# Performance work log

Hardware: AMD Instinct MI355X
Metric: run time of the kernel (lower is better)

The kernel has to match this reference:

```python
import jax, jax.numpy as jnp
import numpy as np

N_NODES = 50000
N_EDGES = 640000
N_GRAPHS = 64
D_IN = 3
D_H = 128
N_CLASSES = 10
EPS = 1e-5


def setup_inputs() -> dict:
    key = jax.random.key(0)
    ks = jax.random.split(key, 32)
    inp = {
        "x": jax.random.normal(ks[0], (N_NODES, D_IN), dtype=jnp.float32),
        "src": jax.random.randint(ks[1], (N_EDGES,), 0, N_NODES, dtype=jnp.int32),
        "dst": jax.random.randint(ks[2], (N_EDGES,), 0, N_NODES, dtype=jnp.int32),
        "batch": jnp.sort(jax.random.randint(ks[3], (N_NODES,), 0, N_GRAPHS, dtype=jnp.int32)),
        "enc_w": jax.random.normal(ks[4], (D_IN, D_H), dtype=jnp.float32) * 0.1,
        "enc_b": jnp.zeros((D_H,), jnp.float32),
        "fc_w": jax.random.normal(ks[5], (D_H, D_H), dtype=jnp.float32) * 0.05,
        "fc_b": jnp.zeros((D_H,), jnp.float32),
        "pred_w": jax.random.normal(ks[6], (D_H, N_CLASSES), dtype=jnp.float32) * 0.05,
        "pred_b": jnp.zeros((N_CLASSES,), jnp.float32),
    }
    for i in range(4):
        inp[f"w{i}"] = jax.random.normal(ks[8 + i], (D_H, D_H), dtype=jnp.float32) * 0.05
        inp[f"b{i}"] = jnp.zeros((D_H,), jnp.float32)
        inp[f"ln_w{i}"] = jnp.ones((D_H,), jnp.float32)
        inp[f"ln_b{i}"] = jnp.zeros((D_H,), jnp.float32)
    return inp


def _gcn_norm(src, dst, n):
    # add self-loops, symmetric deg^{-1/2} normalization (GCNConv default)
    loop = jnp.arange(n, dtype=src.dtype)
    src_f = jnp.concatenate([src, loop])
    dst_f = jnp.concatenate([dst, loop])
    deg = jax.ops.segment_sum(jnp.ones_like(dst_f, jnp.float32), dst_f, num_segments=n)
    dinv = jnp.where(deg > 0, 1.0 / jnp.sqrt(deg), 0.0)
    norm = dinv[src_f] * dinv[dst_f]
    return src_f, dst_f, norm


def _gcn(x, w, b, src_f, dst_f, norm, n):
    h = x @ w                           # [N, D]
    m = h[src_f] * norm[:, None]        # gather + scale  [E+N, D]
    return jax.ops.segment_sum(m, dst_f, num_segments=n) + b


def _graph_ln(x, w, b):
    # PyG LayerNorm mode='graph', batch=None: normalize over ALL nodes+channels
    mu = x.mean()
    sd = jnp.sqrt(((x - mu) ** 2).mean())
    return (x - mu) / (sd + EPS) * w + b


def reference(x, src, dst, batch, enc_w, enc_b, fc_w, fc_b, pred_w, pred_b,
              w0, b0, ln_w0, ln_b0, w1, b1, ln_w1, ln_b1,
              w2, b2, ln_w2, ln_b2, w3, b3, ln_w3, ln_b3):
    n = x.shape[0]
    src_f, dst_f, norm = _gcn_norm(src, dst, n)
    h = jax.nn.elu(x @ enc_w + enc_b)   # input encoder (Linear + ELU)
    convs = [(w0, b0, ln_w0, ln_b0), (w1, b1, ln_w1, ln_b1),
             (w2, b2, ln_w2, ln_b2), (w3, b3, ln_w3, ln_b3)]
    for w, b, lw, lb in convs:
        h = _gcn(h, w, b, src_f, dst_f, norm, n)
        h = jax.nn.relu(h)
        h = _graph_ln(h, lw, lb)
    g = jax.ops.segment_max(h, batch, num_segments=N_GRAPHS)  # global_max_pool
    g = jnp.tanh(g @ fc_w + fc_b)
    return g @ pred_w + pred_b
```

## Files before the change

### kernel.cpp

```cpp
#include <hip/hip_runtime.h>
#include <cfloat>
#include <cmath>

#define D 128
#define D4 32
#define LB 64

typedef __attribute__((ext_vector_type(8))) short short8;
typedef __attribute__((ext_vector_type(4))) float f32x4;

__device__ __forceinline__ float4 f4fma(float s, float4 a, float4 acc) {
    acc.x = fmaf(s, a.x, acc.x);
    acc.y = fmaf(s, a.y, acc.y);
    acc.z = fmaf(s, a.z, acc.z);
    acc.w = fmaf(s, a.w, acc.w);
    return acc;
}

__device__ __forceinline__ unsigned short f2bf(float x) {
    unsigned int b = __float_as_uint(x);
    unsigned int r = (b + 0x7FFFu + ((b >> 16) & 1u)) >> 16;
    return (unsigned short)r;
}

__device__ __forceinline__ unsigned int pack2bf(float a, float b) {
    return (unsigned int)f2bf(a) | ((unsigned int)f2bf(b) << 16);
}

__device__ __forceinline__ float bf2f(unsigned short u) {
    return __uint_as_float(((unsigned int)u) << 16);
}

__device__ __forceinline__ void accum8(float* a, float nrm, uint4 t) {
    a[0] = fmaf(nrm, bf2f((unsigned short)(t.x & 0xFFFFu)), a[0]);
    a[1] = fmaf(nrm, bf2f((unsigned short)(t.x >> 16)), a[1]);
    a[2] = fmaf(nrm, bf2f((unsigned short)(t.y & 0xFFFFu)), a[2]);
    a[3] = fmaf(nrm, bf2f((unsigned short)(t.y >> 16)), a[3]);
    a[4] = fmaf(nrm, bf2f((unsigned short)(t.z & 0xFFFFu)), a[4]);
    a[5] = fmaf(nrm, bf2f((unsigned short)(t.z >> 16)), a[5]);
    a[6] = fmaf(nrm, bf2f((unsigned short)(t.w & 0xFFFFu)), a[6]);
    a[7] = fmaf(nrm, bf2f((unsigned short)(t.w >> 16)), a[7]);
}

__global__ void k_count(const int* __restrict__ dst, int* __restrict__ cnt, int E) {
    int i = blockIdx.x * blockDim.x + threadIdx.x;
    if (i < E) atomicAdd(&cnt[dst[i]], 1);
}

__global__ void k_scan1(const int* __restrict__ cnt, int* __restrict__ bsum, int N) {
    __shared__ int red[256];
    int i = blockIdx.x * 256 + threadIdx.x;
    red[threadIdx.x] = (i < N) ? cnt[i] : 0;
    __syncthreads();
    for (int off = 128; off; off >>= 1) {
        if (threadIdx.x < off) red[threadIdx.x] += red[threadIdx.x + off];
        __syncthreads();
    }
    if (threadIdx.x == 0) bsum[blockIdx.x] = red[0];
}

__global__ void k_scan2(int* __restrict__ bsum, int NB, int* __restrict__ rowptrN) {
    __shared__ int s[256];
    int t = threadIdx.x;
    int v = (t < NB) ? bsum[t] : 0;
    s[t] = v;
    __syncthreads();
    for (int off = 1; off < 256; off <<= 1) {
        int u = (t >= off) ? s[t - off] : 0;
        __syncthreads();
        s[t] += u;
        __syncthreads();
    }
    if (t < NB) bsum[t] = (t == 0) ? 0 : s[t - 1];
    if (t == 255) *rowptrN = s[255];
}

__global__ void k_scan3(const int* __restrict__ cnt, const int* __restrict__ bsum,
                        int* __restrict__ rowptr, int* __restrict__ cur,
                        float* __restrict__ dinv, int N) {
    __shared__ int s[256];
    int i = blockIdx.x * 256 + threadIdx.x;
    int v = (i < N) ? cnt[i] : 0;
    s[threadIdx.x] = v;
    __syncthreads();
    for (int off = 1; off < 256; off <<= 1) {
        int u = (threadIdx.x >= off) ? s[threadIdx.x - off] : 0;
        __syncthreads();
        s[threadIdx.x] += u;
        __syncthreads();
    }
    if (i < N) {
        int excl = ((threadIdx.x == 0) ? 0 : s[threadIdx.x - 1]) + bsum[blockIdx.x];
        rowptr[i] = excl;
        cur[i] = excl;
        dinv[i] = 1.0f / sqrtf((float)v + 1.0f);
    }
}

__global__ void k_fill(const int* __restrict__ src, const int* __restrict__ dst,
                       const float* __restrict__ dinv, int* __restrict__ cur,
                       int2* __restrict__ edata, int E) {
    int e = blockIdx.x * blockDim.x + threadIdx.x;
    if (e >= E) return;
    int s = src[e], d = dst[e];
    int p = atomicAdd(&cur[d], 1);
    edata[p] = make_int2(s, __float_as_int(dinv[s] * dinv[d]));
}

__global__ void k_enc(const float* __restrict__ x, const float* __restrict__ w,
                      const float* __restrict__ b, unsigned short* __restrict__ h, int N) {
    int idx = blockIdx.x * blockDim.x + threadIdx.x;
    if (idx >= N * D4) return;
    int n = idx >> 5, c4 = idx & 31;
    const float4* w4 = (const float4*)w;
    float4 b4 = ((const float4*)b)[c4];
    float x0 = x[n * 3 + 0], x1 = x[n * 3 + 1], x2 = x[n * 3 + 2];
    float4 v = b4;
    v = f4fma(x0, w4[0 * D4 + c4], v);
    v = f4fma(x1, w4[1 * D4 + c4], v);
    v = f4fma(x2, w4[2 * D4 + c4], v);
    v.x = v.x > 0.f ? v.x : expm1f(v.x);
    v.y = v.y > 0.f ? v.y : expm1f(v.y);
    v.z = v.z > 0.f ? v.z : expm1f(v.z);
    v.w = v.w > 0.f ? v.w : expm1f(v.w);
    ushort4 o;
    o.x = f2bf(v.x); o.y = f2bf(v.y); o.z = f2bf(v.z); o.w = f2bf(v.w);
    ((ushort4*)h)[idx] = o;
}

__global__ void k_prep(const float* __restrict__ w, const float* __restrict__ lw,
                       const float* __restrict__ lb, const double* __restrict__ sums,
                       unsigned short* __restrict__ wt, float* __restrict__ konst, int N) {
    __shared__ float sc[D], of[D];
    float mu = 0.f, inv = 1.f;
    if (lw) {
        double M = (double)N * D;
        double m = sums[0] / M;
        double var = sums[1] / M - m * m;
        float sd = sqrtf(var > 0.0 ? (float)var : 0.f);
        inv = 1.f / (sd + 1e-5f);
        mu = (float)m;
    }
    for (int i = threadIdx.x; i < D; i += blockDim.x) {
        float l = lw ? lw[i] : 1.f;
        float s = inv * l;
        sc[i] = s;
        of[i] = (lw ? lb[i] : 0.f) - mu * s;
    }
    __syncthreads();
    if (blockIdx.x < 8) {
        int nl = threadIdx.x & 15;
        int ck = threadIdx.x >> 4;
        int n = blockIdx.x * 16 + nl;
        unsigned int p[4];
        #pragma unroll
        for (int q = 0; q < 4; ++q) {
            int k0 = ck * 8 + 2 * q;
            float v0 = sc[k0 + 0] * w[(k0 + 0) * D + n];
            float v1 = sc[k0 + 1] * w[(k0 + 1) * D + n];
            p[q] = pack2bf(v0, v1);
        }
        uint4 u = make_uint4(p[0], p[1], p[2], p[3]);
        ((uint4*)(wt + (size_t)n * D))[ck] = u;
    } else {
        for (int j = threadIdx.x; j < D; j += blockDim.x) {
            float acc = 0.f;
            for (int c = 0; c < D; ++c) acc = fmaf(of[c], w[c * D + j], acc);
            konst[j] = acc;
        }
    }
}

__launch_bounds__(256)
__global__ void k_layer(const unsigned short* __restrict__ Ain,
                        const unsigned short* __restrict__ wt,
                        const float* __restrict__ konst, const float* __restrict__ bias,
                        const int2* __restrict__ edata, const int* __restrict__ rowptr,
                        const float* __restrict__ dinv,
                        unsigned short* __restrict__ Aout,
                        double* __restrict__ sums, int N) {
    __shared__ uint4 a_lds4[1024];
    __shared__ float rs[LB];
    __shared__ float ss[4], sq[4];
    char* a_lds = (char*)a_lds4;
    int row0 = blockIdx.x * LB;

    int g = threadIdx.x >> 4;
    int lane = threadIdx.x & 15;
    const uint4* T16 = (const uint4*)Ain;
    for (int k = 0; k < 4; ++k) {
        int nl = g * 4 + k;
        int n = row0 + nl;
        if (n < N) {
            int e0 = rowptr[n], e1 = rowptr[n + 1];
            float acc[8];
            #pragma unroll
            for (int q = 0; q < 8; ++q) acc[q] = 0.f;
            float rsum = 0.f;
            int e = e0;
            for (; e + 8 <= e1; e += 8) {
                int2 ed[8]; uint4 tv[8];
                #pragma unroll
                for (int j = 0; j < 8; ++j) ed[j] = edata[e + j];
                #pragma unroll
                for (int j = 0; j < 8; ++j) tv[j] = T16[(size_t)ed[j].x * 16 + lane];
                #pragma unroll
                for (int j = 0; j < 8; ++j) {
                    float nm = __int_as_float(ed[j].y);
                    accum8(acc, nm, tv[j]);
                    rsum += nm;
                }
            }
            for (; e + 4 <= e1; e += 4) {
                int2 ed[4]; uint4 tv[4];
                #pragma unroll
                for (int j = 0; j < 4; ++j) ed[j] = edata[e + j];
                #pragma unroll
                for (int j = 0; j < 4; ++j) tv[j] = T16[(size_t)ed[j].x * 16 + lane];
                #pragma unroll
                for (int j = 0; j < 4; ++j) {
                    float nm = __int_as_float(ed[j].y);
                    accum8(acc, nm, tv[j]);
                    rsum += nm;
                }
            }
            for (; e < e1; ++e) {
                int2 d = edata[e];
                float nm = __int_as_float(d.y);
                accum8(acc, nm, T16[(size_t)d.x * 16 + lane]);
                rsum += nm;
            }
            float di = dinv[n];
            float sl = di * di;
            accum8(acc, sl, T16[(size_t)n * 16 + lane]);
            rsum += sl;
            int i = nl * 16 + lane;
            int byte = (i << 4) ^ ((nl & 7) << 4);
            *(uint4*)(a_lds + byte) = make_uint4(pack2bf(acc[0], acc[1]),
                                                 pack2bf(acc[2], acc[3]),
                                                 pack2bf(acc[4], acc[5]),
                                                 pack2bf(acc[6], acc[7]));
            if (lane == 0) rs[nl] = rsum;
        }
    }
    __syncthreads();

    int wv = threadIdx.x >> 6;
    int l64 = threadIdx.x & 63;
    int lrow = l64 & 15;
    int kg = l64 >> 4;

    f32x4 acc2[8];
    #pragma unroll
    for (int ct = 0; ct < 8; ++ct) acc2[ct] = (f32x4){0.f, 0.f, 0.f, 0.f};

    #pragma unroll
    for (int ks = 0; ks < 4; ++ks) {
        int ar = wv * 16 + lrow;
        int abyte = (ar * 256 + ks * 64 + kg * 16) ^ ((ar & 7) << 4);
        short8 a = *(short8*)(a_lds + abyte);
        #pragma unroll
        for (int ct = 0; ct < 8; ++ct) {
            int wr = ct * 16 + lrow;
            short8 b = *(const short8*)(wt + (size_t)wr * D + ks * 32 + kg * 8);
            acc2[ct] = __builtin_amdgcn_mfma_f32_16x16x32_bf16(a, b, acc2[ct], 0, 0, 0);
        }
    }

    float ls = 0.f, lq = 0.f;
    #pragma unroll
    for (int ct = 0; ct < 8; ++ct) {
        int col = ct * 16 + lrow;
        float kc = konst[col];
        float bb = bias[col];
        #pragma unroll
        for (int r = 0; r < 4; ++r) {
            int rtile = wv * 16 + kg * 4 + r;
            int row = row0 + rtile;
            if (row < N) {
                float v = acc2[ct][r] + rs[rtile] * kc + bb;
                v = fmaxf(v, 0.f);
                Aout[(size_t)row * D + col] = f2bf(v);
                ls += v;
                lq += v * v;
            }
        }
    }
    for (int off = 32; off; off >>= 1) {
        ls += __shfl_down(ls, off);
        lq += __shfl_down(lq, off);
    }
    if (l64 == 0) { ss[wv] = ls; sq[wv] = lq; }
    __syncthreads();
    if (threadIdx.x == 0) {
        float S = ss[0] + ss[1] + ss[2] + ss[3];
        float Q = sq[0] + sq[1] + sq[2] + sq[3];
        atomicAdd(&sums[0], (double)S);
        atomicAdd(&sums[1], (double)Q);
    }
}

__launch_bounds__(512)
__global__ void k_tail(const unsigned short* __restrict__ A, const int* __restrict__ batch,
                       const float* __restrict__ lw, const float* __restrict__ lb,
                       const double* __restrict__ sums,
                       const float* __restrict__ fc_w, const float* __restrict__ fc_b,
                       const float* __restrict__ pred_w, const float* __restrict__ pred_b,
                       float* __restrict__ out, int N) {
    int gi = blockIdx.x;
    int lo = 0, hi = N;
    while (lo < hi) { int mid = (lo + hi) >> 1; if (batch[mid] < gi) lo = mid + 1; else hi = mid; }
    int start = lo;
    hi = N;
    while (lo < hi) { int mid = (lo + hi) >> 1; if (batch[mid] < gi + 1) lo = mid + 1; else hi = mid; }
    int end = lo;

    int c = threadIdx.x & 127, sub = threadIdx.x >> 7;
    double M = (double)N * D;
    double m_ = sums[0] / M;
    double var = sums[1] / M - m_ * m_;
    float sd = sqrtf(var > 0.0 ? (float)var : 0.f);
    float inv = 1.f / (sd + 1e-5f);
    float s = inv * lw[c];
    float o = lb[c] - (float)m_ * s;

    float mx = -FLT_MAX;
    for (int node = start + sub; node < end; node += 4)
        mx = fmaxf(mx, fmaf(bf2f(A[(size_t)node * D + c]), s, o));

    __shared__ float red[4][128];
    __shared__ float gm[128], tr[128];
    red[sub][c] = mx;
    __syncthreads();
    if (sub == 0)
        gm[c] = fmaxf(fmaxf(red[0][c], red[1][c]), fmaxf(red[2][c], red[3][c]));
    __syncthreads();
    if (threadIdx.x < 128) {
        float acc = fc_b[c];
        for (int k = 0; k < D; ++k) acc = fmaf(gm[k], fc_w[k * D + c], acc);
        tr[c] = tanhf(acc);
    }
    __syncthreads();
    if (threadIdx.x < 10) {
        int j = threadIdx.x;
        float acc = pred_b[j];
        for (int k = 0; k < D; ++k) acc = fmaf(tr[k], pred_w[k * 10 + j], acc);
        out[gi * 10 + j] = acc;
    }
}

extern "C" void kernel_launch(void* const* d_in, const int* in_sizes, int n_in,
                              void* d_out, int out_size, void* d_ws, size_t ws_size,
                              hipStream_t stream) {
    const float* x      = (const float*)d_in[0];
    const int*   src    = (const int*)d_in[1];
    const int*   dst    = (const int*)d_in[2];
    const int*   batch  = (const int*)d_in[3];
    const float* enc_w  = (const float*)d_in[4];
    const float* enc_b  = (const float*)d_in[5];
    const float* fc_w   = (const float*)d_in[6];
    const float* fc_b   = (const float*)d_in[7];
    const float* pred_w = (const float*)d_in[8];
    const float* pred_b = (const float*)d_in[9];

    int N = in_sizes[0] / 3;
    int E = in_sizes[1];
    int G = out_size / 10;
    int NB = (N + 255) / 256;

    char* ws = (char*)d_ws;
    size_t off = 0;
    auto align512 = [](size_t v) { return (v + 511) / 512 * 512; };
    int*   cnt    = (int*)(ws + off);   off += align512((size_t)N * 4);
    double* sums  = (double*)(ws + off); off += 512;
    float* dinv   = (float*)(ws + off); off += align512((size_t)N * 4);
    int*   rowptr = (int*)(ws + off);   off += align512(((size_t)N + 1) * 4);
    int*   cur    = (int*)(ws + off);   off += align512((size_t)N * 4);
    int*   bsum   = (int*)(ws + off);   off += align512(1024);
    int2*  edata  = (int2*)(ws + off);  off += align512((size_t)E * 8);
    unsigned short* A0 = (unsigned short*)(ws + off); off += align512((size_t)N * D * 2);
    unsigned short* A1 = (unsigned short*)(ws + off); off += align512((size_t)N * D * 2);
    unsigned short* wt = (unsigned short*)(ws + off); off += align512((size_t)D * D * 2);
    float* konst  = (float*)(ws + off); off += align512((size_t)D * 4);

    hipMemsetAsync(cnt, 0, align512((size_t)N * 4) + 512, stream);
    k_count<<<(E + 255) / 256, 256, 0, stream>>>(dst, cnt, E);
    k_scan1<<<NB, 256, 0, stream>>>(cnt, bsum, N);
    k_scan2<<<1, 256, 0, stream>>>(bsum, NB, rowptr + N);
    k_scan3<<<NB, 256, 0, stream>>>(cnt, bsum, rowptr, cur, dinv, N);
    k_fill<<<(E + 255) / 256, 256, 0, stream>>>(src, dst, dinv, cur, edata, E);

    int tot4 = N * D4;
    k_enc<<<(tot4 + 255) / 256, 256, 0, stream>>>(x, enc_w, enc_b, A0, N);

    int NBL = (N + LB - 1) / LB;
    unsigned short* Ain = A0;
    unsigned short* Aout = A1;
    for (int L = 0; L < 4; ++L) {
        const float* w  = (const float*)d_in[10 + 4 * L];
        const float* b  = (const float*)d_in[11 + 4 * L];
        const float* lwp = L ? (const float*)d_in[12 + 4 * (L - 1)] : nullptr;
        const float* lbp = L ? (const float*)d_in[13 + 4 * (L - 1)] : nullptr;
        k_prep<<<9, 256, 0, stream>>>(w, lwp, lbp, &sums[2 * (L ? L - 1 : 0)], wt, konst, N);
        k_layer<<<NBL, 256, 0, stream>>>(Ain, wt, konst, b, edata, rowptr, dinv,
                                         Aout, &sums[2 * L], N);
        unsigned short* tmp = Ain; Ain = Aout; Aout = tmp;
    }

    const float* lw3 = (const float*)d_in[12 + 4 * 3];
    const float* lb3 = (const float*)d_in[13 + 4 * 3];
    k_tail<<<G, 512, 0, stream>>>(Ain, batch, lw3, lb3, &sums[6],
                                  fc_w, fc_b, pred_w, pred_b, (float*)d_out, N);
}
```

Before: 567.4 us.

## Halve layer block rows and merge three-pass scan into one kernel

The fused GCN layer kernel now handles 32 rows per block instead of 64. The four waves split the MFMA work as two row tiles by two 64-column halves, which doubles the block count and halves LDS use to raise occupancy and parallelism on the gather. The three scan kernels are replaced by one kernel in which each block recomputes its prefix by summing all earlier counts, removing two launches. The cost is redundant quadratic reads of the count array and more repeated weight loads per row.

```diff
diff --git a/kernel.cpp b/kernel.cpp
--- a/kernel.cpp
+++ b/kernel.cpp
@@ -4,7 +4,7 @@
 
 #define D 128
 #define D4 32
-#define LB 64
+#define LB 32
 
 typedef __attribute__((ext_vector_type(8))) short short8;
 typedef __attribute__((ext_vector_type(4))) float f32x4;
@@ -47,54 +47,39 @@
     if (i < E) atomicAdd(&cnt[dst[i]], 1);
 }
 
-__global__ void k_scan1(const int* __restrict__ cnt, int* __restrict__ bsum, int N) {
-    __shared__ int red[256];
-    int i = blockIdx.x * 256 + threadIdx.x;
-    red[threadIdx.x] = (i < N) ? cnt[i] : 0;
+__global__ void k_scanall(const int* __restrict__ cnt, int* __restrict__ rowptr,
+                          int* __restrict__ cur, float* __restrict__ dinv,
+                          int N, int NB) {
+    __shared__ int pre[256];
+    int b = blockIdx.x, t = threadIdx.x;
+    int limit = b * 256;
+    int s = 0;
+    for (int i = t; i < limit; i += 256) s += cnt[i];
+    pre[t] = s;
     __syncthreads();
     for (int off = 128; off; off >>= 1) {
-        if (threadIdx.x < off) red[threadIdx.x] += red[threadIdx.x + off];
+        if (t < off) pre[t] += pre[t + off];
         __syncthreads();
     }
-    if (threadIdx.x == 0) bsum[blockIdx.x] = red[0];
-}
-
-__global__ void k_scan2(int* __restrict__ bsum, int NB, int* __restrict__ rowptrN) {
-    __shared__ int s[256];
-    int t = threadIdx.x;
-    int v = (t < NB) ? bsum[t] : 0;
-    s[t] = v;
+    int base = pre[0];
+    __syncthreads();
+    int i = b * 256 + t;
+    int v = (i < N) ? cnt[i] : 0;
+    pre[t] = v;
     __syncthreads();
     for (int off = 1; off < 256; off <<= 1) {
-        int u = (t >= off) ? s[t - off] : 0;
+        int u = (t >= off) ? pre[t - off] : 0;
         __syncthreads();
-        s[t] += u;
+        pre[t] += u;
         __syncthreads();
     }
-    if (t < NB) bsum[t] = (t == 0) ? 0 : s[t - 1];
-    if (t == 255) *rowptrN = s[255];
-}
-
-__global__ void k_scan3(const int* __restrict__ cnt, const int* __restrict__ bsum,
-                        int* __restrict__ rowptr, int* __restrict__ cur,
-                        float* __restrict__ dinv, int N) {
-    __shared__ int s[256];
-    int i = blockIdx.x * 256 + threadIdx.x;
-    int v = (i < N) ? cnt[i] : 0;
-    s[threadIdx.x] = v;
-    __syncthreads();
-    for (int off = 1; off < 256; off <<= 1) {
-        int u = (threadIdx.x >= off) ? s[threadIdx.x - off] : 0;
-        __syncthreads();
-        s[threadIdx.x] += u;
-        __syncthreads();
-    }
     if (i < N) {
-        int excl = ((threadIdx.x == 0) ? 0 : s[threadIdx.x - 1]) + bsum[blockIdx.x];
+        int excl = base + ((t == 0) ? 0 : pre[t - 1]);
         rowptr[i] = excl;
         cur[i] = excl;
         dinv[i] = 1.0f / sqrtf((float)v + 1.0f);
     }
+    if (b == NB - 1 && t == 255) rowptr[N] = base + pre[255];
 }
 
 __global__ void k_fill(const int* __restrict__ src, const int* __restrict__ dst,
@@ -179,7 +164,7 @@
                         const float* __restrict__ dinv,
                         unsigned short* __restrict__ Aout,
                         double* __restrict__ sums, int N) {
-    __shared__ uint4 a_lds4[1024];
+    __shared__ uint4 a_lds4[512];
     __shared__ float rs[LB];
     __shared__ float ss[4], sq[4];
     char* a_lds = (char*)a_lds4;
@@ -188,8 +173,8 @@
     int g = threadIdx.x >> 4;
     int lane = threadIdx.x & 15;
     const uint4* T16 = (const uint4*)Ain;
-    for (int k = 0; k < 4; ++k) {
-        int nl = g * 4 + k;
+    for (int k = 0; k < 2; ++k) {
+        int nl = g * 2 + k;
         int n = row0 + nl;
         if (n < N) {
             int e0 = rowptr[n], e1 = rowptr[n + 1];
@@ -249,33 +234,35 @@
     int l64 = threadIdx.x & 63;
     int lrow = l64 & 15;
     int kg = l64 >> 4;
-
-    f32x4 acc2[8];
+    int rt = wv & 1;
+    int cb = wv >> 1;
+
+    f32x4 acc2[4];
     #pragma unroll
-    for (int ct = 0; ct < 8; ++ct) acc2[ct] = (f32x4){0.f, 0.f, 0.f, 0.f};
+    for (int ct = 0; ct < 4; ++ct) acc2[ct] = (f32x4){0.f, 0.f, 0.f, 0.f};
 
     #pragma unroll
     for (int ks = 0; ks < 4; ++ks) {
-        int ar = wv * 16 + lrow;
+        int ar = rt * 16 + lrow;
         int abyte = (ar * 256 + ks * 64 + kg * 16) ^ ((ar & 7) << 4);
         short8 a = *(short8*)(a_lds + abyte);
         #pragma unroll
-        for (int ct = 0; ct < 8; ++ct) {
-            int wr = ct * 16 + lrow;
-            short8 b = *(const short8*)(wt + (size_t)wr * D + ks * 32 + kg * 8);
+        for (int ct = 0; ct < 4; ++ct) {
+            int col = cb * 64 + ct * 16 + lrow;
+            short8 b = *(const short8*)(wt + (size_t)col * D + ks * 32 + kg * 8);
             acc2[ct] = __builtin_amdgcn_mfma_f32_16x16x32_bf16(a, b, acc2[ct], 0, 0, 0);
         }
     }
 
     float ls = 0.f, lq = 0.f;
     #pragma unroll
-    for (int ct = 0; ct < 8; ++ct) {
-        int col = ct * 16 + lrow;
+    for (int ct = 0; ct < 4; ++ct) {
+        int col = cb * 64 + ct * 16 + lrow;
         float kc = konst[col];
         float bb = bias[col];
         #pragma unroll
         for (int r = 0; r < 4; ++r) {
-            int rtile = wv * 16 + kg * 4 + r;
+            int rtile = rt * 16 + kg * 4 + r;
             int row = row0 + rtile;
             if (row < N) {
                 float v = acc2[ct][r] + rs[rtile] * kc + bb;
@@ -376,7 +363,6 @@
     float* dinv   = (float*)(ws + off); off += align512((size_t)N * 4);
     int*   rowptr = (int*)(ws + off);   off += align512(((size_t)N + 1) * 4);
     int*   cur    = (int*)(ws + off);   off += align512((size_t)N * 4);
-    int*   bsum   = (int*)(ws + off);   off += align512(1024);
     int2*  edata  = (int2*)(ws + off);  off += align512((size_t)E * 8);
     unsigned short* A0 = (unsigned short*)(ws + off); off += align512((size_t)N * D * 2);
     unsigned short* A1 = (unsigned short*)(ws + off); off += align512((size_t)N * D * 2);
@@ -385,9 +371,7 @@
 
     hipMemsetAsync(cnt, 0, align512((size_t)N * 4) + 512, stream);
     k_count<<<(E + 255) / 256, 256, 0, stream>>>(dst, cnt, E);
-    k_scan1<<<NB, 256, 0, stream>>>(cnt, bsum, N);
-    k_scan2<<<1, 256, 0, stream>>>(bsum, NB, rowptr + N);
-    k_scan3<<<NB, 256, 0, stream>>>(cnt, bsum, rowptr, cur, dinv, N);
+    k_scanall<<<NB, 256, 0, stream>>>(cnt, rowptr, cur, dinv, N, NB);
     k_fill<<<(E + 255) / 256, 256, 0, stream>>>(src, dst, dinv, cur, edata, E);
 
     int tot4 = N * D4;
```

Result: faster. 540.1 us (-4.8%).
